# Performance work log

Hardware: AMD Instinct MI355X
Metric: run time of the kernel (lower is better)

## Reference

```python
import jax, jax.numpy as jnp
import numpy as np
from jax import lax

B, T, C = 32, 512, 128
K = 3                      # top_k periods
MIN_P, MAX_P = 8, 64       # period search band
P_MAX = MAX_P              # grid width
CYC_MAX = (T + MIN_P - 1) // MIN_P
KW = 9                     # cyc-axis depthwise kernel
GN_G = 32                  # _best_gn_groups(128)
EPS_GN = 1e-5
EPS_ORTH = 1e-6
EPS_W = 1e-8


def setup_inputs() -> dict:
    key = jax.random.key(0)
    ks = jax.random.split(key, 4)
    return {
        "x": jax.random.normal(ks[0], (B, T, C), jnp.float32),
        "W_dw": jax.random.normal(ks[1], (C, 1, KW), jnp.float32) * 0.1,
        "W_pw": jax.random.normal(ks[2], (C, C), jnp.float32) * (1.0 / np.sqrt(C)),
        "gn_weight": jnp.ones((C,), jnp.float32),
        "gn_bias": jnp.zeros((C,), jnp.float32),
        "W_gate": jax.random.normal(ks[3], (C, C), jnp.float32) * (1.0 / np.sqrt(C)),
        "gamma": jnp.full((C,), 1e-3, jnp.float32),
    }


def _autocorr_topk(x):
    # x: [B,T,C] -> period idx [B,K], softmax weights [B,K]
    Xf = jnp.fft.rfft(x, axis=1)
    Pm = (Xf * jnp.conj(Xf)).real.mean(-1)          # [B, T//2+1]
    r = jnp.fft.irfft(Pm, n=T, axis=1)              # [B, T] autocorrelation
    lag = jnp.arange(T)
    valid = (lag >= MIN_P) & (lag <= MAX_P)
    very_neg = jnp.finfo(x.dtype).min / 8
    rm = jnp.where(valid[None, :], r, very_neg)
    vals, idx = lax.top_k(rm, K)
    w = jax.nn.softmax(vals, axis=1)
    return idx, w


def _fold(s, p):
    # s: [N,T,C], p: [N] int periods -> Z [N,C,CYC_MAX,P_MAX], mask, unfold index maps
    N = s.shape[0]
    p = jnp.maximum(p, 1)
    tpad = ((T + p - 1) // p) * p                   # [N]
    cyc = jnp.arange(CYC_MAX)[None, :, None]
    pos = jnp.arange(P_MAX)[None, None, :]
    time = cyc * p[:, None, None] + pos             # [N,CYC_MAX,P_MAX]
    valid = (pos < p[:, None, None]) & (time < tpad[:, None, None])
    # right-side reflect padding indices
    m = 2 * (T - 1)
    rr = time % m
    src_idx = jnp.where(rr < T, rr, m - rr)
    src = jnp.take_along_axis(s, src_idx.reshape(N, -1)[:, :, None], axis=1)
    src = src.reshape(N, CYC_MAX, P_MAX, C) * valid[..., None].astype(s.dtype)
    Z = jnp.transpose(src, (0, 3, 1, 2))            # [N,C,CYC_MAX,P_MAX]
    mask2d = valid[:, None].astype(s.dtype)         # [N,1,CYC_MAX,P_MAX]
    t = jnp.arange(T)[None, :]
    cyc_T = jnp.clip(t // p[:, None], 0, CYC_MAX - 1)
    pos_T = jnp.clip(t % p[:, None], 0, P_MAX - 1)
    return Z, mask2d, cyc_T, pos_T


def _cyc_conv(Z, mask2d, W_dw, W_pw, gn_w, gn_b, W_gate, gamma):
    # CycAxisConv1d: mean over period axis, depthwise+pointwise conv along cyc,
    # GroupNorm, GELU, SE-gate, LayerScale residual broadcast back to 2D.
    N, _, L, _ = Z.shape
    u = Z.mean(-1)                                  # [N,C,L]
    h = lax.conv_general_dilated(u, W_dw, (1,), [(KW // 2, KW // 2)],
                                 dimension_numbers=('NCH', 'OIH', 'NCH'),
                                 feature_group_count=C)
    h = jnp.einsum('oc,ncl->nol', W_pw, h)
    hg = h.reshape(N, GN_G, C // GN_G, L)
    mean = hg.mean((2, 3), keepdims=True)
    var = hg.var((2, 3), keepdims=True)
    hg = (hg - mean) * lax.rsqrt(var + EPS_GN)
    h = hg.reshape(N, C, L) * gn_w[None, :, None] + gn_b[None, :, None]
    h = jax.nn.gelu(h, approximate=False)
    gate = jax.nn.sigmoid(jnp.einsum('oc,nc->no', W_gate, u.mean(-1)))
    h = h * gate[:, :, None]
    x2d = h[..., None] * gamma[None, :, None, None] * mask2d
    return Z + x2d


def _unfold(Z, cyc_T, pos_T):
    N = Z.shape[0]
    Zf = Z.reshape(N, C, CYC_MAX * P_MAX)
    sp = jnp.clip(cyc_T * P_MAX + pos_T, 0, CYC_MAX * P_MAX - 1)  # [N,T]
    y = jnp.take_along_axis(Zf, sp[:, None, :], axis=2)           # [N,C,T]
    return jnp.transpose(y, (0, 2, 1))                            # [N,T,C]


def reference(x, W_dw, W_pw, gn_weight, gn_bias, W_gate, gamma):
    idx, w = _autocorr_topk(x)                      # [B,K], [B,K]
    p_flat = idx.reshape(-1)                        # [B*K]
    s = jnp.repeat(x, K, axis=0)                    # [B*K,T,C]
    Z, mask2d, cyc_T, pos_T = _fold(s, p_flat)
    Z = _cyc_conv(Z, mask2d, W_dw, W_pw, gn_weight, gn_bias, W_gate, gamma)
    y = _unfold(Z, cyc_T, pos_T).reshape(B, K, T, C)
    periodic = jnp.einsum('bk,bktc->btc', w, y)
    # period confidence Gamma from weight entropy
    H = -(w * jnp.log(w + EPS_W)).sum(1)
    Gamma = jnp.clip(1.0 - H / (jnp.log(float(K) + EPS_W) + EPS_W), 0.0, 1.0)
    # orthogonal residual of local part against periodic part
    local = x - periodic
    num = (local * periodic).sum(1, keepdims=True)
    den = (periodic * periodic).sum(1, keepdims=True) + EPS_ORTH
    local_orth = local - num / den * periodic
    g = Gamma[:, None, None]
    return g * (periodic + local_orth) + (1.0 - g) * x
```

## Files before the change

### kernel.cpp

```cpp
#include <hip/hip_runtime.h>
#include <math.h>

static constexpr int Bn   = 32;
static constexpr int Tn   = 512;
static constexpr int Cn   = 128;
static constexpr int Kk   = 3;
static constexpr int NLAG = 57;
static constexpr int CYC  = 64;
static constexpr int KWn  = 9;

__global__ __launch_bounds__(256) void k_autocorr(const float* __restrict__ x,
    float* __restrict__ r_ws) {
  const int b   = blockIdx.x >> 3;
  const int grp = blockIdx.x & 7;
  const int L0  = 8 + grp * 8;
  const int tid = threadIdx.x;
  const float4* X4 = (const float4*)(x + (size_t)b * Tn * Cn);

  float acc[8];
#pragma unroll
  for (int i = 0; i < 8; ++i) acc[i] = 0.f;

  for (int it = 0; it < 8; ++it) {
    const int id = it * 256 + tid;
    const int c4 = id & 31;
    const int t0 = (id >> 5) * 8;
    float4 A[8];
#pragma unroll
    for (int j = 0; j < 8; ++j) A[j] = X4[(t0 + j) * 32 + c4];
    float4 R[16];
#pragma unroll
    for (int j = 0; j < 16; ++j) R[j] = X4[((t0 + L0 + j) & 511) * 32 + c4];
#pragma unroll
    for (int g = 0; g < 8; ++g) {
#pragma unroll
      for (int j = 0; j < 8; ++j) {
        const float4 a = A[j];
        const float4 r = R[g + j];
        acc[g] += a.x * r.x + a.y * r.y + a.z * r.z + a.w * r.w;
      }
    }
  }

  __shared__ float lds_r[4][8];
  const int lane = tid & 63, wave = tid >> 6;
#pragma unroll
  for (int g = 0; g < 8; ++g) {
    float v = acc[g];
#pragma unroll
    for (int m = 32; m > 0; m >>= 1) v += __shfl_xor(v, m, 64);
    if (lane == 0) lds_r[wave][g] = v;
  }
  __syncthreads();
  if (tid < 8) {
    const int li = grp * 8 + tid;
    if (li < NLAG) {
      r_ws[b * NLAG + li] =
          (lds_r[0][tid] + lds_r[1][tid] + lds_r[2][tid] + lds_r[3][tid]) * (1.0f / Cn);
    }
  }
}

__global__ __launch_bounds__(64) void k_topk(const float* __restrict__ r_ws,
    int* __restrict__ p_idx, float* __restrict__ wv, float* __restrict__ gval) {
  const int b = blockIdx.x;
  const int tid = threadIdx.x;
  __shared__ float rs[NLAG];
  if (tid < NLAG) rs[tid] = r_ws[b * NLAG + tid];
  __syncthreads();
  if (tid == 0) {
    float tmp[NLAG];
    for (int i = 0; i < NLAG; ++i) tmp[i] = rs[i];
    float vals[Kk]; int lags[Kk];
    for (int k = 0; k < Kk; ++k) {
      float best = -INFINITY; int bi = 0;
      for (int i = 0; i < NLAG; ++i)
        if (tmp[i] > best) { best = tmp[i]; bi = i; }
      vals[k] = best; lags[k] = bi + 8; tmp[bi] = -INFINITY;
    }
    const float m  = vals[0];
    const float e0 = expf(vals[0] - m), e1 = expf(vals[1] - m), e2 = expf(vals[2] - m);
    const float s  = e0 + e1 + e2;
    const float w0 = e0 / s, w1 = e1 / s, w2 = e2 / s;
    p_idx[b * 3 + 0] = lags[0]; p_idx[b * 3 + 1] = lags[1]; p_idx[b * 3 + 2] = lags[2];
    wv[b * 3 + 0] = w0; wv[b * 3 + 1] = w1; wv[b * 3 + 2] = w2;
    const float H  = -(w0 * logf(w0 + 1e-8f) + w1 * logf(w1 + 1e-8f) + w2 * logf(w2 + 1e-8f));
    const float lg = logf(3.0f + 1e-8f) + 1e-8f;
    float G = 1.0f - H / lg;
    gval[b] = fminf(fmaxf(G, 0.0f), 1.0f);
  }
}

__global__ __launch_bounds__(128) void k_fold_u(const float* __restrict__ x,
    const int* __restrict__ p_idx, float* __restrict__ u) {
  const int l = blockIdx.x;
  const int n = blockIdx.y;
  const int c = threadIdx.x;
  const int p = p_idx[n];
  const int ncyc = (Tn + p - 1) / p;
  float acc = 0.f;
  if (l < ncyc) {
    const float* xb = x + (size_t)(n / 3) * Tn * Cn;
    const int base = l * p;
    for (int j = 0; j < p; ++j) {
      const int time = base + j;
      const int src = time < Tn ? time : (2 * (Tn - 1) - time);
      acc += xb[src * Cn + c];
    }
  }
  u[((size_t)n * CYC + l) * Cn + c] = acc * (1.0f / 64.0f);
}

__global__ __launch_bounds__(256) void k_cycconv(
    const float* __restrict__ u, const float* __restrict__ Wdw,
    const float* __restrict__ Wpw, const float* __restrict__ gnw,
    const float* __restrict__ gnb, const float* __restrict__ Wgate,
    float* __restrict__ hh) {
  const int n  = blockIdx.x;
  const int og = blockIdx.y;
  const int tid = threadIdx.x;
  const int l  = tid & 63;
  const int wq = __builtin_amdgcn_readfirstlane(tid >> 6);

  __shared__ float smem[8320];
  __shared__ float ubar_s[Cn];
  __shared__ float gates_s[16];

  const float* un = u + (size_t)n * CYC * Cn;

  for (int i = 0; i < 32; ++i) {
    const int idx = i * 256 + tid;
    const int ll = idx >> 7, cc = idx & 127;
    smem[ll * 129 + cc] = un[idx];
  }
  __syncthreads();

  if (tid < Cn) {
    float s = 0.f;
    for (int ll = 0; ll < CYC; ++ll) s += smem[ll * 129 + tid];
    ubar_s[tid] = s * (1.0f / CYC);
  }

  float hreg[32];
  {
    const int c0 = wq * 32;
#pragma unroll
    for (int i = 0; i < 32; ++i) {
      const int c = c0 + i;
      float s = 0.f;
#pragma unroll
      for (int k = 0; k < KWn; ++k) {
        const int ll = l + k - KWn / 2;
        if (ll >= 0 && ll < CYC) s += smem[ll * 129 + c] * Wdw[c * KWn + k];
      }
      hreg[i] = s;
    }
  }
  __syncthreads();

  if (tid < 16) {
    const int o = og * 16 + tid;
    float z = 0.f;
    for (int c = 0; c < Cn; ++c) z += Wgate[o * Cn + c] * ubar_s[c];
    gates_s[tid] = 1.0f / (1.0f + expf(-z));
  }

  {
    const int c0 = wq * 32;
#pragma unroll
    for (int i = 0; i < 32; ++i) smem[(c0 + i) * 65 + l] = hreg[i];
  }
  __syncthreads();

  const int o4 = og * 16 + wq * 4;
  float acc[4];
#pragma unroll
  for (int i = 0; i < 4; ++i) acc[i] = 0.f;
  const float* wb = Wpw + (size_t)o4 * Cn;
  for (int c = 0; c < Cn; ++c) {
    const float hv = smem[c * 65 + l];
#pragma unroll
    for (int i = 0; i < 4; ++i) acc[i] = fmaf(wb[i * Cn + c], hv, acc[i]);
  }

  float s1 = acc[0] + acc[1] + acc[2] + acc[3];
  float s2 = acc[0]*acc[0] + acc[1]*acc[1] + acc[2]*acc[2] + acc[3]*acc[3];
#pragma unroll
  for (int m = 32; m > 0; m >>= 1) {
    s1 += __shfl_xor(s1, m, 64);
    s2 += __shfl_xor(s2, m, 64);
  }
  const float mean = s1 * (1.0f / 256.0f);
  const float var  = s2 * (1.0f / 256.0f) - mean * mean;
  const float rstd = rsqrtf(var + 1e-5f);

  float4 res;
  float* rp = (float*)&res;
#pragma unroll
  for (int i = 0; i < 4; ++i) {
    const int o = o4 + i;
    float h = (acc[i] - mean) * rstd;
    h = h * gnw[o] + gnb[o];
    h = 0.5f * h * (1.0f + erff(h * 0.70710678118654752440f));
    rp[i] = h * gates_s[o - og * 16];
  }
  *(float4*)(hh + (size_t)n * CYC * Cn + l * Cn + o4) = res;
}

__global__ __launch_bounds__(128) void k_dot(const float* __restrict__ x,
    const float* __restrict__ hh, const int* __restrict__ p_idx,
    const float* __restrict__ wv, const float* __restrict__ gamma,
    float* __restrict__ pna, float* __restrict__ pda) {
  const int q = blockIdx.x, b = blockIdx.y;
  const int tid = threadIdx.x;
  const int t0 = q * 64;
  __shared__ unsigned short cycs[64][4];

  const int p0 = p_idx[b * 3 + 0], p1 = p_idx[b * 3 + 1], p2 = p_idx[b * 3 + 2];
  const float w0 = wv[b * 3 + 0], w1 = wv[b * 3 + 1], w2 = wv[b * 3 + 2];
  const float sw = w0 + w1 + w2;
  if (tid < 64) {
    const int t = t0 + tid;
    cycs[tid][0] = (unsigned short)(t / p0);
    cycs[tid][1] = (unsigned short)(t / p1);
    cycs[tid][2] = (unsigned short)(t / p2);
  }
  __syncthreads();

  const int c = tid;
  const float gam = gamma[c];
  const float* hh0 = hh + ((size_t)(b * 3 + 0) * CYC) * Cn + c;
  const float* hh1 = hh + ((size_t)(b * 3 + 1) * CYC) * Cn + c;
  const float* hh2 = hh + ((size_t)(b * 3 + 2) * CYC) * Cn + c;
  const float* xb = x + (size_t)b * Tn * Cn;

  float na = 0.f, da = 0.f;
  for (int tt = 0; tt < 64; ++tt) {
    const int t = t0 + tt;
    const float xv = xb[t * Cn + c];
    const float dv = gam * (w0 * hh0[cycs[tt][0] * Cn] +
                            w1 * hh1[cycs[tt][1] * Cn] +
                            w2 * hh2[cycs[tt][2] * Cn]);
    const float P = sw * xv + dv;
    na += (xv - P) * P;
    da += P * P;
  }
  pna[((size_t)b * 8 + q) * Cn + c] = na;
  pda[((size_t)b * 8 + q) * Cn + c] = da;
}

__global__ __launch_bounds__(128) void k_out(const float* __restrict__ x,
    const float* __restrict__ hh, const int* __restrict__ p_idx,
    const float* __restrict__ wv, const float* __restrict__ gval,
    const float* __restrict__ gamma, const float* __restrict__ pna,
    const float* __restrict__ pda, float* __restrict__ out) {
  const int q = blockIdx.x, b = blockIdx.y;
  const int tid = threadIdx.x;
  const int t0 = q * 64;
  __shared__ unsigned short cycs[64][4];

  const int p0 = p_idx[b * 3 + 0], p1 = p_idx[b * 3 + 1], p2 = p_idx[b * 3 + 2];
  const float w0 = wv[b * 3 + 0], w1 = wv[b * 3 + 1], w2 = wv[b * 3 + 2];
  const float sw = w0 + w1 + w2;
  const float g = gval[b];
  if (tid < 64) {
    const int t = t0 + tid;
    cycs[tid][0] = (unsigned short)(t / p0);
    cycs[tid][1] = (unsigned short)(t / p1);
    cycs[tid][2] = (unsigned short)(t / p2);
  }
  __syncthreads();

  const int c = tid;
  float num = 0.f, den = 1e-6f;
#pragma unroll
  for (int qq = 0; qq < 8; ++qq) {
    num += pna[((size_t)b * 8 + qq) * Cn + c];
    den += pda[((size_t)b * 8 + qq) * Cn + c];
  }
  const float sc = g * (num / den);

  const float gam = gamma[c];
  const float* hh0 = hh + ((size_t)(b * 3 + 0) * CYC) * Cn + c;
  const float* hh1 = hh + ((size_t)(b * 3 + 1) * CYC) * Cn + c;
  const float* hh2 = hh + ((size_t)(b * 3 + 2) * CYC) * Cn + c;
  const float* xb = x + (size_t)b * Tn * Cn;
  float* ob = out + (size_t)b * Tn * Cn;

  for (int tt = 0; tt < 64; ++tt) {
    const int t = t0 + tt;
    const float xv = xb[t * Cn + c];
    const float dv = gam * (w0 * hh0[cycs[tt][0] * Cn] +
                            w1 * hh1[cycs[tt][1] * Cn] +
                            w2 * hh2[cycs[tt][2] * Cn]);
    const float P = sw * xv + dv;
    ob[t * Cn + c] = xv - sc * P;
  }
}

extern "C" void kernel_launch(void* const* d_in, const int* in_sizes, int n_in,
                              void* d_out, int out_size, void* d_ws, size_t ws_size,
                              hipStream_t stream) {
  const float* x     = (const float*)d_in[0];
  const float* Wdw   = (const float*)d_in[1];
  const float* Wpw   = (const float*)d_in[2];
  const float* gnw   = (const float*)d_in[3];
  const float* gnb   = (const float*)d_in[4];
  const float* Wgate = (const float*)d_in[5];
  const float* gamma = (const float*)d_in[6];
  float* out = (float*)d_out;

  char* ws = (char*)d_ws;
  int*   p_idx = (int*)ws;
  float* wvp   = (float*)(ws + 512);
  float* gvalp = (float*)(ws + 1024);
  float* r_ws  = (float*)(ws + 2048);
  float* pna   = (float*)(ws + 10240);
  float* pda   = (float*)(ws + 10240 + 131072);
  float* u     = (float*)(ws + 10240 + 262144);
  float* hh    = (float*)(ws + 10240 + 262144 + 3145728);

  k_autocorr<<<Bn * 8, 256, 0, stream>>>(x, r_ws);
  k_topk<<<Bn, 64, 0, stream>>>(r_ws, p_idx, wvp, gvalp);
  k_fold_u<<<dim3(CYC, Bn * Kk), 128, 0, stream>>>(x, p_idx, u);
  k_cycconv<<<dim3(Bn * Kk, 8), 256, 0, stream>>>(u, Wdw, Wpw, gnw, gnb, Wgate, hh);
  k_dot<<<dim3(8, Bn), 128, 0, stream>>>(x, hh, p_idx, wvp, gamma, pna, pda);
  k_out<<<dim3(8, Bn), 128, 0, stream>>>(x, hh, p_idx, wvp, gvalp, gamma, pna, pda, out);
}
```

Baseline: 166.2 us.

## Fuse pipeline into three kernels with wave-parallel top-k and LDS-cached periodic term

Collapses six launches into three. Top-k selection moves into the consumer kernels as a wave-shuffle argmax, so the single-thread top-k kernel goes away. Folding, depthwise conv, pointwise conv, GroupNorm and gating now run in one 512-thread block per (batch, k), so the fold buffer is no longer written to and read back from global memory. The dot and output stages merge into one kernel per (batch, 16-channel group) that keeps the periodic term in shared memory and does a single pass over x and hh, removing the partial-sum arrays. In exchange, each batch element now runs with far fewer blocks (96 and 256), the top-k work is repeated in every block, and the large per-block LDS footprint may limit occupancy.

Result: faster. 150.7 us (-9.3%).

```diff
diff --git a/kernel.cpp b/kernel.cpp
--- a/kernel.cpp
+++ b/kernel.cpp
@@ -4,15 +4,14 @@
 static constexpr int Bn   = 32;
 static constexpr int Tn   = 512;
 static constexpr int Cn   = 128;
-static constexpr int Kk   = 3;
 static constexpr int NLAG = 57;
 static constexpr int CYC  = 64;
-static constexpr int KWn  = 9;
 
 __global__ __launch_bounds__(256) void k_autocorr(const float* __restrict__ x,
     float* __restrict__ r_ws) {
-  const int b   = blockIdx.x >> 3;
-  const int grp = blockIdx.x & 7;
+  const int w   = (blockIdx.x & 7) * 32 + (blockIdx.x >> 3);
+  const int b   = w >> 3;
+  const int grp = w & 7;
   const int L0  = 8 + grp * 8;
   const int tid = threadIdx.x;
   const float4* X4 = (const float4*)(x + (size_t)b * Tn * Cn);
@@ -61,240 +60,249 @@
   }
 }
 
-__global__ __launch_bounds__(64) void k_topk(const float* __restrict__ r_ws,
-    int* __restrict__ p_idx, float* __restrict__ wv, float* __restrict__ gval) {
-  const int b = blockIdx.x;
-  const int tid = threadIdx.x;
-  __shared__ float rs[NLAG];
-  if (tid < NLAG) rs[tid] = r_ws[b * NLAG + tid];
-  __syncthreads();
-  if (tid == 0) {
-    float tmp[NLAG];
-    for (int i = 0; i < NLAG; ++i) tmp[i] = rs[i];
-    float vals[Kk]; int lags[Kk];
-    for (int k = 0; k < Kk; ++k) {
-      float best = -INFINITY; int bi = 0;
-      for (int i = 0; i < NLAG; ++i)
-        if (tmp[i] > best) { best = tmp[i]; bi = i; }
-      vals[k] = best; lags[k] = bi + 8; tmp[bi] = -INFINITY;
-    }
-    const float m  = vals[0];
-    const float e0 = expf(vals[0] - m), e1 = expf(vals[1] - m), e2 = expf(vals[2] - m);
-    const float s  = e0 + e1 + e2;
-    const float w0 = e0 / s, w1 = e1 / s, w2 = e2 / s;
-    p_idx[b * 3 + 0] = lags[0]; p_idx[b * 3 + 1] = lags[1]; p_idx[b * 3 + 2] = lags[2];
-    wv[b * 3 + 0] = w0; wv[b * 3 + 1] = w1; wv[b * 3 + 2] = w2;
-    const float H  = -(w0 * logf(w0 + 1e-8f) + w1 * logf(w1 + 1e-8f) + w2 * logf(w2 + 1e-8f));
-    const float lg = logf(3.0f + 1e-8f) + 1e-8f;
-    float G = 1.0f - H / lg;
-    gval[b] = fminf(fmaxf(G, 0.0f), 1.0f);
-  }
-}
-
-__global__ __launch_bounds__(128) void k_fold_u(const float* __restrict__ x,
-    const int* __restrict__ p_idx, float* __restrict__ u) {
-  const int l = blockIdx.x;
-  const int n = blockIdx.y;
-  const int c = threadIdx.x;
-  const int p = p_idx[n];
+__global__ __launch_bounds__(512) void k_fold_conv(
+    const float* __restrict__ x, const float* __restrict__ r_ws,
+    const float* __restrict__ Wdw, const float* __restrict__ Wpw,
+    const float* __restrict__ gnw, const float* __restrict__ gnb,
+    const float* __restrict__ Wgate, float* __restrict__ hh) {
+  const int n  = (blockIdx.x & 7) * 12 + (blockIdx.x >> 3);
+  const int b  = n / 3, kk = n % 3;
+  const int tid  = threadIdx.x;
+  const int lane = tid & 63;
+  const int wq   = __builtin_amdgcn_readfirstlane(tid >> 6);
+
+  __shared__ float su[CYC * 129];
+  __shared__ float sh[Cn * 65];
+  __shared__ float ubar_s[Cn];
+  __shared__ float gates_s[Cn];
+  __shared__ int   p_sh;
+
+  if (tid < 64) {
+    const float* rb = r_ws + b * NLAG;
+    float v  = (tid < NLAG) ? rb[tid] : -INFINITY;
+    int  idx = tid;
+    int  lag = 8;
+#pragma unroll
+    for (int k = 0; k < 3; ++k) {
+      if (k > kk) break;
+      float bv = v; int bi = idx;
+#pragma unroll
+      for (int m = 32; m > 0; m >>= 1) {
+        const float ov = __shfl_xor(bv, m, 64);
+        const int   oi = __shfl_xor(bi, m, 64);
+        if (ov > bv || (ov == bv && oi < bi)) { bv = ov; bi = oi; }
+      }
+      lag = bi + 8;
+      if (idx == bi) v = -INFINITY;
+    }
+    if (tid == 0) p_sh = lag;
+  }
+  __syncthreads();
+  const int p    = p_sh;
   const int ncyc = (Tn + p - 1) / p;
-  float acc = 0.f;
-  if (l < ncyc) {
-    const float* xb = x + (size_t)(n / 3) * Tn * Cn;
-    const int base = l * p;
-    for (int j = 0; j < p; ++j) {
-      const int time = base + j;
-      const int src = time < Tn ? time : (2 * (Tn - 1) - time);
-      acc += xb[src * Cn + c];
-    }
-  }
-  u[((size_t)n * CYC + l) * Cn + c] = acc * (1.0f / 64.0f);
-}
-
-__global__ __launch_bounds__(256) void k_cycconv(
-    const float* __restrict__ u, const float* __restrict__ Wdw,
-    const float* __restrict__ Wpw, const float* __restrict__ gnw,
-    const float* __restrict__ gnb, const float* __restrict__ Wgate,
-    float* __restrict__ hh) {
-  const int n  = blockIdx.x;
-  const int og = blockIdx.y;
-  const int tid = threadIdx.x;
-  const int l  = tid & 63;
-  const int wq = __builtin_amdgcn_readfirstlane(tid >> 6);
-
-  __shared__ float smem[8320];
-  __shared__ float ubar_s[Cn];
-  __shared__ float gates_s[16];
-
-  const float* un = u + (size_t)n * CYC * Cn;
-
-  for (int i = 0; i < 32; ++i) {
-    const int idx = i * 256 + tid;
-    const int ll = idx >> 7, cc = idx & 127;
-    smem[ll * 129 + cc] = un[idx];
+
+  {
+    const int l  = tid >> 3;
+    const int c0 = (tid & 7) * 16;
+    float a[16];
+#pragma unroll
+    for (int i = 0; i < 16; ++i) a[i] = 0.f;
+    if (l < ncyc) {
+      const float4* xb4 = (const float4*)(x + (size_t)b * Tn * Cn) + (c0 >> 2);
+      const int base = l * p;
+      for (int j = 0; j < p; ++j) {
+        const int time = base + j;
+        const int src  = time < Tn ? time : (2 * (Tn - 1) - time);
+        const float4 v0 = xb4[src * 32 + 0];
+        const float4 v1 = xb4[src * 32 + 1];
+        const float4 v2 = xb4[src * 32 + 2];
+        const float4 v3 = xb4[src * 32 + 3];
+        a[0]  += v0.x; a[1]  += v0.y; a[2]  += v0.z; a[3]  += v0.w;
+        a[4]  += v1.x; a[5]  += v1.y; a[6]  += v1.z; a[7]  += v1.w;
+        a[8]  += v2.x; a[9]  += v2.y; a[10] += v2.z; a[11] += v2.w;
+        a[12] += v3.x; a[13] += v3.y; a[14] += v3.z; a[15] += v3.w;
+      }
+    }
+    float* dst = su + l * 129 + c0;
+#pragma unroll
+    for (int i = 0; i < 16; ++i) dst[i] = a[i] * (1.0f / 64.0f);
   }
   __syncthreads();
 
   if (tid < Cn) {
     float s = 0.f;
-    for (int ll = 0; ll < CYC; ++ll) s += smem[ll * 129 + tid];
+    for (int l = 0; l < CYC; ++l) s += su[l * 129 + tid];
     ubar_s[tid] = s * (1.0f / CYC);
   }
 
-  float hreg[32];
   {
-    const int c0 = wq * 32;
-#pragma unroll
-    for (int i = 0; i < 32; ++i) {
+    const int c0 = wq * 16;
+#pragma unroll
+    for (int i = 0; i < 16; ++i) {
       const int c = c0 + i;
       float s = 0.f;
 #pragma unroll
-      for (int k = 0; k < KWn; ++k) {
-        const int ll = l + k - KWn / 2;
-        if (ll >= 0 && ll < CYC) s += smem[ll * 129 + c] * Wdw[c * KWn + k];
-      }
-      hreg[i] = s;
-    }
-  }
-  __syncthreads();
-
-  if (tid < 16) {
-    const int o = og * 16 + tid;
+      for (int k = 0; k < 9; ++k) {
+        const int ll = lane + k - 4;
+        if (ll >= 0 && ll < CYC) s += su[ll * 129 + c] * Wdw[c * 9 + k];
+      }
+      sh[c * 65 + lane] = s;
+    }
+  }
+  __syncthreads();
+
+  {
+    const int ol   = lane & 15;
+    const int part = lane >> 4;
+    const int o    = wq * 16 + ol;
     float z = 0.f;
-    for (int c = 0; c < Cn; ++c) z += Wgate[o * Cn + c] * ubar_s[c];
-    gates_s[tid] = 1.0f / (1.0f + expf(-z));
-  }
-
+    const float* wg = Wgate + (size_t)o * Cn + part * 32;
+    const float* ub = ubar_s + part * 32;
+    for (int c = 0; c < 32; ++c) z += wg[c] * ub[c];
+    z += __shfl_xor(z, 16, 64);
+    z += __shfl_xor(z, 32, 64);
+    if (part == 0) gates_s[o] = 1.0f / (1.0f + expf(-z));
+  }
+
+  float acc[16];
+#pragma unroll
+  for (int i = 0; i < 16; ++i) acc[i] = 0.f;
+  const int o0 = wq * 16;
   {
-    const int c0 = wq * 32;
-#pragma unroll
-    for (int i = 0; i < 32; ++i) smem[(c0 + i) * 65 + l] = hreg[i];
-  }
-  __syncthreads();
-
-  const int o4 = og * 16 + wq * 4;
-  float acc[4];
-#pragma unroll
-  for (int i = 0; i < 4; ++i) acc[i] = 0.f;
-  const float* wb = Wpw + (size_t)o4 * Cn;
-  for (int c = 0; c < Cn; ++c) {
-    const float hv = smem[c * 65 + l];
-#pragma unroll
-    for (int i = 0; i < 4; ++i) acc[i] = fmaf(wb[i * Cn + c], hv, acc[i]);
-  }
-
-  float s1 = acc[0] + acc[1] + acc[2] + acc[3];
-  float s2 = acc[0]*acc[0] + acc[1]*acc[1] + acc[2]*acc[2] + acc[3]*acc[3];
-#pragma unroll
-  for (int m = 32; m > 0; m >>= 1) {
-    s1 += __shfl_xor(s1, m, 64);
-    s2 += __shfl_xor(s2, m, 64);
-  }
-  const float mean = s1 * (1.0f / 256.0f);
-  const float var  = s2 * (1.0f / 256.0f) - mean * mean;
-  const float rstd = rsqrtf(var + 1e-5f);
-
-  float4 res;
-  float* rp = (float*)&res;
-#pragma unroll
-  for (int i = 0; i < 4; ++i) {
-    const int o = o4 + i;
-    float h = (acc[i] - mean) * rstd;
-    h = h * gnw[o] + gnb[o];
-    h = 0.5f * h * (1.0f + erff(h * 0.70710678118654752440f));
-    rp[i] = h * gates_s[o - og * 16];
-  }
-  *(float4*)(hh + (size_t)n * CYC * Cn + l * Cn + o4) = res;
+    const float* wb = Wpw + (size_t)o0 * Cn;
+    for (int c = 0; c < Cn; ++c) {
+      const float hv = sh[c * 65 + lane];
+#pragma unroll
+      for (int i = 0; i < 16; ++i) acc[i] = fmaf(wb[i * Cn + c], hv, acc[i]);
+    }
+  }
+  __syncthreads();
+
+  float4 res[4];
+#pragma unroll
+  for (int g = 0; g < 4; ++g) {
+    float s1 = acc[4*g] + acc[4*g+1] + acc[4*g+2] + acc[4*g+3];
+    float s2 = acc[4*g]*acc[4*g] + acc[4*g+1]*acc[4*g+1]
+             + acc[4*g+2]*acc[4*g+2] + acc[4*g+3]*acc[4*g+3];
+#pragma unroll
+    for (int m = 32; m > 0; m >>= 1) {
+      s1 += __shfl_xor(s1, m, 64);
+      s2 += __shfl_xor(s2, m, 64);
+    }
+    const float mean = s1 * (1.0f / 256.0f);
+    const float var  = s2 * (1.0f / 256.0f) - mean * mean;
+    const float rstd = rsqrtf(var + 1e-5f);
+    float* rp = (float*)&res[g];
+#pragma unroll
+    for (int i = 0; i < 4; ++i) {
+      const int o = o0 + 4*g + i;
+      float h = (acc[4*g + i] - mean) * rstd;
+      h = h * gnw[o] + gnb[o];
+      h = 0.5f * h * (1.0f + erff(h * 0.70710678118654752440f));
+      rp[i] = h * gates_s[o];
+    }
+  }
+  float4* hp = (float4*)(hh + (size_t)n * CYC * Cn + (size_t)lane * Cn + o0);
+#pragma unroll
+  for (int g = 0; g < 4; ++g) hp[g] = res[g];
 }
 
-__global__ __launch_bounds__(128) void k_dot(const float* __restrict__ x,
-    const float* __restrict__ hh, const int* __restrict__ p_idx,
-    const float* __restrict__ wv, const float* __restrict__ gamma,
-    float* __restrict__ pna, float* __restrict__ pda) {
-  const int q = blockIdx.x, b = blockIdx.y;
+__global__ __launch_bounds__(128) void k_dot_out(
+    const float* __restrict__ x, const float* __restrict__ hh,
+    const float* __restrict__ r_ws, const float* __restrict__ gamma,
+    float* __restrict__ out) {
+  const int b  = blockIdx.x;
+  const int cg = blockIdx.y;
   const int tid = threadIdx.x;
-  const int t0 = q * 64;
-  __shared__ unsigned short cycs[64][4];
-
-  const int p0 = p_idx[b * 3 + 0], p1 = p_idx[b * 3 + 1], p2 = p_idx[b * 3 + 2];
-  const float w0 = wv[b * 3 + 0], w1 = wv[b * 3 + 1], w2 = wv[b * 3 + 2];
+  const int c_l = tid & 15;
+  const int tg  = tid >> 4;
+  const int c   = cg * 16 + c_l;
+
+  __shared__ float P_s[Tn * 16];
+  __shared__ unsigned short cyc_s[Tn][3];
+  __shared__ float params[4];
+  __shared__ int   pp[3];
+  __shared__ float red[2][2][16];
+  __shared__ float sc_s[16];
+
+  if (tid < 64) {
+    const float* rb = r_ws + b * NLAG;
+    float v  = (tid < NLAG) ? rb[tid] : -INFINITY;
+    int  idx = tid;
+    float vals[3]; int lags[3];
+#pragma unroll
+    for (int k = 0; k < 3; ++k) {
+      float bv = v; int bi = idx;
+#pragma unroll
+      for (int m = 32; m > 0; m >>= 1) {
+        const float ov = __shfl_xor(bv, m, 64);
+        const int   oi = __shfl_xor(bi, m, 64);
+        if (ov > bv || (ov == bv && oi < bi)) { bv = ov; bi = oi; }
+      }
+      vals[k] = bv; lags[k] = bi + 8;
+      if (idx == bi) v = -INFINITY;
+    }
+    if (tid == 0) {
+      const float m  = vals[0];
+      const float e0 = expf(vals[0] - m), e1 = expf(vals[1] - m), e2 = expf(vals[2] - m);
+      const float s  = e0 + e1 + e2;
+      const float w0 = e0 / s, w1 = e1 / s, w2 = e2 / s;
+      pp[0] = lags[0]; pp[1] = lags[1]; pp[2] = lags[2];
+      params[0] = w0; params[1] = w1; params[2] = w2;
+      const float H  = -(w0 * logf(w0 + 1e-8f) + w1 * logf(w1 + 1e-8f) + w2 * logf(w2 + 1e-8f));
+      const float lg = logf(3.0f + 1e-8f) + 1e-8f;
+      params[3] = fminf(fmaxf(1.0f - H / lg, 0.0f), 1.0f);
+    }
+  }
+  __syncthreads();
+  const int p0 = pp[0], p1 = pp[1], p2 = pp[2];
+  const float w0 = params[0], w1 = params[1], w2 = params[2];
+  const float g  = params[3];
   const float sw = w0 + w1 + w2;
-  if (tid < 64) {
-    const int t = t0 + tid;
-    cycs[tid][0] = (unsigned short)(t / p0);
-    cycs[tid][1] = (unsigned short)(t / p1);
-    cycs[tid][2] = (unsigned short)(t / p2);
-  }
-  __syncthreads();
-
-  const int c = tid;
+
+  for (int t = tid; t < Tn; t += 128) {
+    cyc_s[t][0] = (unsigned short)(t / p0);
+    cyc_s[t][1] = (unsigned short)(t / p1);
+    cyc_s[t][2] = (unsigned short)(t / p2);
+  }
+  __syncthreads();
+
   const float gam = gamma[c];
-  const float* hh0 = hh + ((size_t)(b * 3 + 0) * CYC) * Cn + c;
-  const float* hh1 = hh + ((size_t)(b * 3 + 1) * CYC) * Cn + c;
-  const float* hh2 = hh + ((size_t)(b * 3 + 2) * CYC) * Cn + c;
   const float* xb = x + (size_t)b * Tn * Cn;
+  const float* h0 = hh + (size_t)(b * 3 + 0) * CYC * Cn + c;
+  const float* h1 = hh + (size_t)(b * 3 + 1) * CYC * Cn + c;
+  const float* h2 = hh + (size_t)(b * 3 + 2) * CYC * Cn + c;
 
   float na = 0.f, da = 0.f;
   for (int tt = 0; tt < 64; ++tt) {
-    const int t = t0 + tt;
+    const int t = (tg << 6) + tt;
     const float xv = xb[t * Cn + c];
-    const float dv = gam * (w0 * hh0[cycs[tt][0] * Cn] +
-                            w1 * hh1[cycs[tt][1] * Cn] +
-                            w2 * hh2[cycs[tt][2] * Cn]);
+    const float dv = gam * (w0 * h0[cyc_s[t][0] * Cn] +
+                            w1 * h1[cyc_s[t][1] * Cn] +
+                            w2 * h2[cyc_s[t][2] * Cn]);
     const float P = sw * xv + dv;
+    P_s[t * 16 + c_l] = P;
     na += (xv - P) * P;
     da += P * P;
   }
-  pna[((size_t)b * 8 + q) * Cn + c] = na;
-  pda[((size_t)b * 8 + q) * Cn + c] = da;
-}
-
-__global__ __launch_bounds__(128) void k_out(const float* __restrict__ x,
-    const float* __restrict__ hh, const int* __restrict__ p_idx,
-    const float* __restrict__ wv, const float* __restrict__ gval,
-    const float* __restrict__ gamma, const float* __restrict__ pna,
-    const float* __restrict__ pda, float* __restrict__ out) {
-  const int q = blockIdx.x, b = blockIdx.y;
-  const int tid = threadIdx.x;
-  const int t0 = q * 64;
-  __shared__ unsigned short cycs[64][4];
-
-  const int p0 = p_idx[b * 3 + 0], p1 = p_idx[b * 3 + 1], p2 = p_idx[b * 3 + 2];
-  const float w0 = wv[b * 3 + 0], w1 = wv[b * 3 + 1], w2 = wv[b * 3 + 2];
-  const float sw = w0 + w1 + w2;
-  const float g = gval[b];
-  if (tid < 64) {
-    const int t = t0 + tid;
-    cycs[tid][0] = (unsigned short)(t / p0);
-    cycs[tid][1] = (unsigned short)(t / p1);
-    cycs[tid][2] = (unsigned short)(t / p2);
-  }
-  __syncthreads();
-
-  const int c = tid;
-  float num = 0.f, den = 1e-6f;
-#pragma unroll
-  for (int qq = 0; qq < 8; ++qq) {
-    num += pna[((size_t)b * 8 + qq) * Cn + c];
-    den += pda[((size_t)b * 8 + qq) * Cn + c];
-  }
-  const float sc = g * (num / den);
-
-  const float gam = gamma[c];
-  const float* hh0 = hh + ((size_t)(b * 3 + 0) * CYC) * Cn + c;
-  const float* hh1 = hh + ((size_t)(b * 3 + 1) * CYC) * Cn + c;
-  const float* hh2 = hh + ((size_t)(b * 3 + 2) * CYC) * Cn + c;
-  const float* xb = x + (size_t)b * Tn * Cn;
+  na += __shfl_xor(na, 16, 64); da += __shfl_xor(da, 16, 64);
+  na += __shfl_xor(na, 32, 64); da += __shfl_xor(da, 32, 64);
+  const int wv_ = tid >> 6;
+  if ((tid & 63) < 16) { red[0][wv_][c_l] = na; red[1][wv_][c_l] = da; }
+  __syncthreads();
+  if (tid < 16) {
+    const float num = red[0][0][tid] + red[0][1][tid];
+    const float den = red[1][0][tid] + red[1][1][tid] + 1e-6f;
+    sc_s[tid] = g * (num / den);
+  }
+  __syncthreads();
+  const float sc = sc_s[c_l];
+
   float* ob = out + (size_t)b * Tn * Cn;
-
   for (int tt = 0; tt < 64; ++tt) {
-    const int t = t0 + tt;
+    const int t = (tg << 6) + tt;
     const float xv = xb[t * Cn + c];
-    const float dv = gam * (w0 * hh0[cycs[tt][0] * Cn] +
-                            w1 * hh1[cycs[tt][1] * Cn] +
-                            w2 * hh2[cycs[tt][2] * Cn]);
-    const float P = sw * xv + dv;
-    ob[t * Cn + c] = xv - sc * P;
+    ob[t * Cn + c] = xv - sc * P_s[t * 16 + c_l];
   }
 }
 
@@ -311,19 +319,10 @@
   float* out = (float*)d_out;
 
   char* ws = (char*)d_ws;
-  int*   p_idx = (int*)ws;
-  float* wvp   = (float*)(ws + 512);
-  float* gvalp = (float*)(ws + 1024);
-  float* r_ws  = (float*)(ws + 2048);
-  float* pna   = (float*)(ws + 10240);
-  float* pda   = (float*)(ws + 10240 + 131072);
-  float* u     = (float*)(ws + 10240 + 262144);
-  float* hh    = (float*)(ws + 10240 + 262144 + 3145728);
+  float* r_ws = (float*)ws;
+  float* hh   = (float*)(ws + 8192);
 
   k_autocorr<<<Bn * 8, 256, 0, stream>>>(x, r_ws);
-  k_topk<<<Bn, 64, 0, stream>>>(r_ws, p_idx, wvp, gvalp);
-  k_fold_u<<<dim3(CYC, Bn * Kk), 128, 0, stream>>>(x, p_idx, u);
-  k_cycconv<<<dim3(Bn * Kk, 8), 256, 0, stream>>>(u, Wdw, Wpw, gnw, gnb, Wgate, hh);
-  k_dot<<<dim3(8, Bn), 128, 0, stream>>>(x, hh, p_idx, wvp, gamma, pna, pda);
-  k_out<<<dim3(8, Bn), 128, 0, stream>>>(x, hh, p_idx, wvp, gvalp, gamma, pna, pda, out);
+  k_fold_conv<<<Bn * 3, 512, 0, stream>>>(x, r_ws, Wdw, Wpw, gnw, gnb, Wgate, hh);
+  k_dot_out<<<dim3(Bn, 8), 128, 0, stream>>>(x, hh, r_ws, gamma, out);
 }
```
